# Optimization experiments

Hardware: AMD Instinct MI355X
Metric: run time of the kernel (lower is better)

## Reference

```python
import jax, jax.numpy as jnp
import numpy as np

B, T, C, L = 64, 1000, 128, 100  # batch, frames, classes (blank=C-1), max label len
NEG = jnp.float32(-1e30)


def setup_inputs() -> dict:
    key = jax.random.key(0)
    k0, k1, k2, k3 = jax.random.split(key, 4)
    # ctc_batch_cost expects softmax probabilities
    y_pred = jax.nn.softmax(jax.random.normal(k0, (B, T, C), dtype=jnp.float32), axis=-1)
    y_true = jax.random.randint(k1, (B, L), 0, C - 1).astype(jnp.int32)  # labels exclude blank
    label_lengths = jax.random.randint(k2, (B,), L // 2, L + 1).astype(jnp.int32)
    input_lengths = jax.random.randint(k3, (B,), T // 2, T + 1).astype(jnp.int32)
    return {"y_true": y_true, "y_pred": y_pred,
            "input_lengths": input_lengths, "label_lengths": label_lengths}


def _ctc_loss(y_true, y_pred, input_lengths, label_lengths):
    # Keras: logits = log(y_pred + epsilon), blank index = C-1
    logp = jnp.log(y_pred + 1e-7)                     # [B,T,C]
    blank = C - 1
    S = 2 * L + 1
    # extended label sequence: blank, l1, blank, l2, ..., blank  -> [B,S]
    ext = jnp.full((B, S), blank, dtype=jnp.int32).at[:, 1::2].set(y_true)
    # gather per-extended-position log probs: [B,T,S]
    logp_ext = jnp.take_along_axis(logp, jnp.broadcast_to(ext[:, None, :], (B, T, S)), axis=2)
    # skip (s-2) transition allowed when ext[s] != blank and ext[s] != ext[s-2]
    ext_m2 = jnp.concatenate([jnp.full((B, 2), blank, jnp.int32), ext[:, :-2]], axis=1)
    skip = (ext != blank) & (ext != ext_m2)           # [B,S]

    alpha0 = jnp.full((B, S), NEG, dtype=logp.dtype)
    alpha0 = alpha0.at[:, 0].set(logp_ext[:, 0, 0]).at[:, 1].set(logp_ext[:, 0, 1])

    def step(alpha, xs):
        lp_t, t = xs                                   # lp_t [B,S]
        a1 = jnp.concatenate([jnp.full((B, 1), NEG, alpha.dtype), alpha[:, :-1]], axis=1)
        a2 = jnp.concatenate([jnp.full((B, 2), NEG, alpha.dtype), alpha[:, :-2]], axis=1)
        a2 = jnp.where(skip, a2, NEG)
        new = jnp.logaddexp(jnp.logaddexp(alpha, a1), a2) + lp_t
        # freeze alpha past each sample's input length
        alpha = jnp.where(t < input_lengths[:, None], new, alpha)
        return alpha, None

    xs = (jnp.moveaxis(logp_ext, 1, 0)[1:], jnp.arange(1, T))
    alpha, _ = jax.lax.scan(step, alpha0, xs)
    # final positions: S_b-1 = 2*label_len, S_b-2 = 2*label_len - 1
    a_last = jnp.take_along_axis(alpha, (2 * label_lengths)[:, None], axis=1)[:, 0]
    a_prev = jnp.take_along_axis(alpha, (2 * label_lengths - 1)[:, None], axis=1)[:, 0]
    return -jnp.logaddexp(a_last, a_prev)[:, None]     # [B,1] like ctc_batch_cost


def reference(y_true, y_pred, input_lengths, label_lengths):
    return _ctc_loss(y_true, y_pred, input_lengths, label_lengths)
```

## Files before the change

kernel.cpp:

```cpp
#include <hip/hip_runtime.h>

#define B_ 64
#define T_ 1000
#define C_ 128
#define L_ 100
#define BLANK 127
#define LN2F 0.69314718055994530942f
#define PH 32
#define FSTRIDE 1024
#define BUFSZ (PH * FSTRIDE)

__device__ __forceinline__ float flog2(float x) { return __builtin_amdgcn_logf(x); }
__device__ __forceinline__ float frcp(float x)  { return __builtin_amdgcn_rcpf(x); }

#define DPP_ROW_SHR1   0x111
#define DPP_ROW_SHR2   0x112
#define DPP_ROW_SHR4   0x114
#define DPP_ROW_SHR8   0x118
#define DPP_WAVE_SHR1  0x138
#define DPP_WAVE_SHL1  0x130

template <int CTRL>
__device__ __forceinline__ int dpp_mov(int src) {
    return __builtin_amdgcn_update_dpp(0, src, CTRL, 0xF, 0xF, false);
}

__global__ __launch_bounds__(320) void ctc_split_kernel(
    const int* __restrict__ y_true, const float* __restrict__ y_pred,
    const int* __restrict__ in_len, const int* __restrict__ lab_len,
    double* __restrict__ AVf, double* __restrict__ AVb,
    double* __restrict__ Ls, int* __restrict__ Es)
{
    const int bb    = blockIdx.x & 63;
    const bool isB  = blockIdx.x >= 64;
    const int tid   = threadIdx.x;
    const int l     = tid & 63;
    const int wv    = tid >> 6;

    __shared__ __align__(16) char ldsb[2 * BUFSZ + 64];
    __shared__ float lgs[2][4];

    const int k1 = min(2 * l, L_ - 1);
    const int k3 = min(2 * l + 1, L_ - 1);
    const int e1 = y_true[bb * L_ + k1];
    const int e3 = y_true[bb * L_ + k3];
    const double m1 = (k1 == 0 || e1 != y_true[bb * L_ + k1 - 1]) ? 1.0 : 0.0;
    const double m3 = (e3 != y_true[bb * L_ + k3 - 1]) ? 1.0 : 0.0;
    const int k1n = min(2 * l + 2, L_ - 1);
    const double m1n = (y_true[bb * L_ + k1n] != y_true[bb * L_ + k1n - 1]) ? 1.0 : 0.0;

    const int Teff = min(T_, in_len[bb]);
    const int N    = Teff - 1;
    const int Hf   = (N + 1) >> 1;
    const int Hb   = N - Hf;
    const int steps_total = isB ? Hb : Hf;
    const int P_full = steps_total >> 5;
    const int rem    = steps_total & 31;
    const int P      = P_full + (rem ? 1 : 0);
    const float* rowb = y_pred + (size_t)bb * T_ * C_;

    double a0 = 0.0, a1 = 0.0, a2 = 0.0, a3 = 0.0;
    double Lsum = 0.0;
    int E = 0;

    const int fs = (wv - 1) * 8;

    auto fillw = [&](int phf) {
        char* bbw = ldsb + (phf & 1) * BUFSZ;
        const int kb_ = phf * PH + fs;
        float g10,g30,gb0, g11,g31,gb1, g12,g32,gb2, g13,g33,gb3,
              g14,g34,gb4, g15,g35,gb5, g16,g36,gb6, g17,g37,gb7;
        int t0_,t1_,t2_,t3_,t4_,t5_,t6_,t7_;
#define FR(i_) (isB ? (N - (kb_ + i_)) : (1 + kb_ + i_))
        t0_=FR(0); t1_=FR(1); t2_=FR(2); t3_=FR(3);
        t4_=FR(4); t5_=FR(5); t6_=FR(6); t7_=FR(7);
#undef FR
        {
            const float* r_;
            r_ = rowb + (size_t)min(max(t0_,1),N) * C_; g10=r_[e1]; g30=r_[e3]; gb0=r_[BLANK];
            r_ = rowb + (size_t)min(max(t1_,1),N) * C_; g11=r_[e1]; g31=r_[e3]; gb1=r_[BLANK];
            r_ = rowb + (size_t)min(max(t2_,1),N) * C_; g12=r_[e1]; g32=r_[e3]; gb2=r_[BLANK];
            r_ = rowb + (size_t)min(max(t3_,1),N) * C_; g13=r_[e1]; g33=r_[e3]; gb3=r_[BLANK];
            r_ = rowb + (size_t)min(max(t4_,1),N) * C_; g14=r_[e1]; g34=r_[e3]; gb4=r_[BLANK];
            r_ = rowb + (size_t)min(max(t5_,1),N) * C_; g15=r_[e1]; g35=r_[e3]; gb5=r_[BLANK];
            r_ = rowb + (size_t)min(max(t6_,1),N) * C_; g16=r_[e1]; g36=r_[e3]; gb6=r_[BLANK];
            r_ = rowb + (size_t)min(max(t7_,1),N) * C_; g17=r_[e1]; g37=r_[e3]; gb7=r_[BLANK];
        }
        __builtin_amdgcn_sched_barrier(0);
        float lgs_ = 0.f;
#define PWR(i_, T_V, G1, G3, GB) { \
        float rb_ = GB + 1e-7f; \
        float rc_ = frcp(rb_); \
        char* q_ = bbw + ((kb_ & 31) + i_) * FSTRIDE; \
        *(double2*)(q_ + 16 * l) = make_double2((double)((G1 + 1e-7f) * rc_), \
                                                 (double)((G3 + 1e-7f) * rc_)); \
        bool ok_ = isB ? (T_V >= Hf + 1 && T_V <= N) : (T_V >= 1 && T_V <= Hf); \
        lgs_ += ok_ ? flog2(rb_) : 0.f; }
        PWR(0, t0_, g10, g30, gb0); PWR(1, t1_, g11, g31, gb1);
        PWR(2, t2_, g12, g32, gb2); PWR(3, t3_, g13, g33, gb3);
        PWR(4, t4_, g14, g34, gb4); PWR(5, t5_, g15, g35, gb5);
        PWR(6, t6_, g16, g36, gb6); PWR(7, t7_, g17, g37, gb7);
#undef PWR
        if (l == 0) lgs[phf & 1][wv - 1] = lgs_;
    };

#define DECLF(Pr) double Pr##q1, Pr##q3
#define DECLB(Pr) double Pr##q1, Pr##q3, Pr##q1n
#define LDF(Pr, fi_) { \
    double2 v_ = *(const double2*)(bbp_ + (fi_) * FSTRIDE + 16 * l); \
    Pr##q1 = v_.x; Pr##q3 = v_.y; }
#define LDFB(Pr, fi_) { \
    double2 v_ = *(const double2*)(bbp_ + (fi_) * FSTRIDE + 16 * l); \
    Pr##q1 = v_.x; Pr##q3 = v_.y; \
    Pr##q1n = *(const double*)(bbp_ + (fi_) * FSTRIDE + 16 * ((l + 1) & 63)); }

#define STEPQ(Pr) { \
    int slo_ = dpp_mov<DPP_WAVE_SHR1>(__double2loint(a3)); \
    int shi_ = dpp_mov<DPP_WAVE_SHR1>(__double2hiint(a3)); \
    double pm1_ = __hiloint2double(shi_, slo_); \
    double n0_ = a0 + pm1_; \
    double n1_ = (a1 + a0 + m1 * pm1_) * Pr##q1; \
    double n2_ = a2 + a1; \
    double n3_ = (a3 + a2 + m3 * a1) * Pr##q3; \
    a0 = n0_; a1 = n1_; a2 = n2_; a3 = n3_; }

#define STEPB(Pr) { \
    int n0lo_ = dpp_mov<DPP_WAVE_SHL1>(__double2loint(a0)); \
    int n0hi_ = dpp_mov<DPP_WAVE_SHL1>(__double2hiint(a0)); \
    int n1lo_ = dpp_mov<DPP_WAVE_SHL1>(__double2loint(a1)); \
    int n1hi_ = dpp_mov<DPP_WAVE_SHL1>(__double2hiint(a1)); \
    double b0n_ = __hiloint2double(n0hi_, n0lo_); \
    double b1n_ = __hiloint2double(n1hi_, n1lo_); \
    double c1_ = a1 * Pr##q1; \
    double c3_ = a3 * Pr##q3; \
    double c1n_ = b1n_ * Pr##q1n; \
    double n0_ = a0 + c1_; \
    double n1_ = c1_ + a2 + m3 * c3_; \
    double n2_ = a2 + c3_; \
    double n3_ = c3_ + b0n_ + m1n * c1n_; \
    a0 = n0_; a1 = n1_; a2 = n2_; a3 = n3_; }

#define DPPMAX(u_, ctrl_) { unsigned t_ = (unsigned)dpp_mov<ctrl_>((int)(u_)); \
    u_ = max(u_, t_); }
#define RESCALE() { \
    unsigned u_ = max(max((unsigned)__double2hiint(a0), (unsigned)__double2hiint(a1)), \
                      max((unsigned)__double2hiint(a2), (unsigned)__double2hiint(a3))); \
    DPPMAX(u_, DPP_ROW_SHR1); \
    DPPMAX(u_, DPP_ROW_SHR2); \
    DPPMAX(u_, DPP_ROW_SHR4); \
    DPPMAX(u_, DPP_ROW_SHR8); \
    unsigned g_ = max(max((unsigned)__builtin_amdgcn_readlane((int)u_, 15), \
                          (unsigned)__builtin_amdgcn_readlane((int)u_, 31)), \
                      max((unsigned)__builtin_amdgcn_readlane((int)u_, 47), \
                          (unsigned)__builtin_amdgcn_readlane((int)u_, 63))); \
    int kk_ = (int)(g_ >> 20); \
    if (kk_ > 0) { \
        double f_ = __hiloint2double((2046 - kk_) << 20, 0); \
        a0 *= f_; a1 *= f_; a2 *= f_; a3 *= f_; \
        E += kk_ - 1023; } }

    if (wv >= 1) {
        fillw(0);
    } else if (!isB) {
        __builtin_amdgcn_s_setprio(1);
        float pb0_ = rowb[BLANK] + 1e-7f;
        float p10_ = rowb[e1]    + 1e-7f;
        a0 = (l == 0) ? 1.0 : 0.0;
        a1 = (l == 0) ? (double)(p10_ / pb0_) : 0.0;
        Lsum = (double)flog2(pb0_);
    } else {
        __builtin_amdgcn_s_setprio(1);
        const int llb = lab_len[bb];
        const int pa = 2 * llb, pq = 2 * llb - 1;
        a0 = (4 * l     == pa) ? 1.0 : 0.0;
        a1 = (4 * l + 1 == pq) ? 1.0 : 0.0;
        a2 = (4 * l + 2 == pa) ? 1.0 : 0.0;
        a3 = (4 * l + 3 == pq) ? 1.0 : 0.0;
    }
    __syncthreads();

    for (int ph = 0; ph < P; ++ph) {
        if (wv >= 1) {
            if (ph + 1 < P) fillw(ph + 1);
        } else {
            const char* bbp_ = ldsb + (ph & 1) * BUFSZ;
            const int steps = (ph < P_full) ? 32 : rem;
            if (!isB) {
                if (steps == 32) {
                    DECLF(A0); DECLF(A1); DECLF(A2); DECLF(A3);
                    DECLF(B0); DECLF(B1); DECLF(B2); DECLF(B3);
                    LDF(A0,0); LDF(A1,1); LDF(A2,2); LDF(A3,3);
                    LDF(B0,4); LDF(B1,5); LDF(B2,6); LDF(B3,7);
                    { STEPQ(A0); STEPQ(A1); STEPQ(A2); STEPQ(A3); }
                    LDF(A0,8); LDF(A1,9); LDF(A2,10); LDF(A3,11);
                    { STEPQ(B0); STEPQ(B1); STEPQ(B2); STEPQ(B3); }
                    LDF(B0,12); LDF(B1,13); LDF(B2,14); LDF(B3,15);
                    { STEPQ(A0); STEPQ(A1); STEPQ(A2); STEPQ(A3); }
                    LDF(A0,16); LDF(A1,17); LDF(A2,18); LDF(A3,19);
                    { STEPQ(B0); STEPQ(B1); STEPQ(B2); STEPQ(B3); } RESCALE();
                    LDF(B0,20); LDF(B1,21); LDF(B2,22); LDF(B3,23);
                    { STEPQ(A0); STEPQ(A1); STEPQ(A2); STEPQ(A3); }
                    LDF(A0,24); LDF(A1,25); LDF(A2,26); LDF(A3,27);
                    { STEPQ(B0); STEPQ(B1); STEPQ(B2); STEPQ(B3); }
                    LDF(B0,28); LDF(B1,29); LDF(B2,30); LDF(B3,31);
                    { STEPQ(A0); STEPQ(A1); STEPQ(A2); STEPQ(A3); }
                    { STEPQ(B0); STEPQ(B1); STEPQ(B2); STEPQ(B3); } RESCALE();
                } else {
                    for (int k_ = 0; k_ < steps; ++k_) {
                        DECLF(Tq); LDF(Tq, k_); STEPQ(Tq);
                        if (k_ == 15) RESCALE();
                    }
                    RESCALE();
                }
            } else {
                if (steps == 32) {
                    DECLB(A0); DECLB(A1); DECLB(A2); DECLB(A3);
                    DECLB(B0); DECLB(B1); DECLB(B2); DECLB(B3);
                    LDFB(A0,0); LDFB(A1,1); LDFB(A2,2); LDFB(A3,3);
                    LDFB(B0,4); LDFB(B1,5); LDFB(B2,6); LDFB(B3,7);
                    { STEPB(A0); STEPB(A1); STEPB(A2); STEPB(A3); }
                    LDFB(A0,8); LDFB(A1,9); LDFB(A2,10); LDFB(A3,11);
                    { STEPB(B0); STEPB(B1); STEPB(B2); STEPB(B3); }
                    LDFB(B0,12); LDFB(B1,13); LDFB(B2,14); LDFB(B3,15);
                    { STEPB(A0); STEPB(A1); STEPB(A2); STEPB(A3); }
                    LDFB(A0,16); LDFB(A1,17); LDFB(A2,18); LDFB(A3,19);
                    { STEPB(B0); STEPB(B1); STEPB(B2); STEPB(B3); } RESCALE();
                    LDFB(B0,20); LDFB(B1,21); LDFB(B2,22); LDFB(B3,23);
                    { STEPB(A0); STEPB(A1); STEPB(A2); STEPB(A3); }
                    LDFB(A0,24); LDFB(A1,25); LDFB(A2,26); LDFB(A3,27);
                    { STEPB(B0); STEPB(B1); STEPB(B2); STEPB(B3); }
                    LDFB(B0,28); LDFB(B1,29); LDFB(B2,30); LDFB(B3,31);
                    { STEPB(A0); STEPB(A1); STEPB(A2); STEPB(A3); }
                    { STEPB(B0); STEPB(B1); STEPB(B2); STEPB(B3); } RESCALE();
                } else {
                    for (int k_ = 0; k_ < steps; ++k_) {
                        DECLB(Tq); LDFB(Tq, k_); STEPB(Tq);
                        if (k_ == 15) RESCALE();
                    }
                    RESCALE();
                }
            }
            Lsum += (double)(lgs[ph & 1][0] + lgs[ph & 1][1] +
                             lgs[ph & 1][2] + lgs[ph & 1][3]);
        }
        __syncthreads();
    }

    if (wv == 0) {
        double* AV = (isB ? AVb : AVf) + bb * 256;
        AV[4 * l + 0] = a0; AV[4 * l + 1] = a1;
        AV[4 * l + 2] = a2; AV[4 * l + 3] = a3;
        if (l == 0) {
            Ls[bb * 2 + (isB ? 1 : 0)] = Lsum;
            Es[bb * 2 + (isB ? 1 : 0)] = E;
        }
    }
}

__global__ __launch_bounds__(64) void ctc_combine_kernel(
    const double* __restrict__ AVf, const double* __restrict__ AVb,
    const double* __restrict__ Ls, const int* __restrict__ Es,
    float* __restrict__ out)
{
    const int b = blockIdx.x;
    const int l = threadIdx.x;
    const double* f = AVf + b * 256;
    const double* g = AVb + b * 256;
    double d = f[4*l+0]*g[4*l+0] + f[4*l+1]*g[4*l+1]
             + f[4*l+2]*g[4*l+2] + f[4*l+3]*g[4*l+3];
    d += __shfl_xor(d, 1);  d += __shfl_xor(d, 2);  d += __shfl_xor(d, 4);
    d += __shfl_xor(d, 8);  d += __shfl_xor(d, 16); d += __shfl_xor(d, 32);
    if (l == 0) {
        double Ltot = Ls[b * 2] + Ls[b * 2 + 1];
        int    Etot = Es[b * 2] + Es[b * 2 + 1];
        int hi = __double2hiint(d), lo = __double2loint(d);
        int ke = (hi >> 20) & 0x7FF;
        double mant = __hiloint2double((hi & 0x000FFFFF) | (1023 << 20), lo);
        float r = flog2((float)mant) + (float)(ke - 1023 + Etot) + (float)Ltot;
        out[b] = -r * LN2F;
    }
}

extern "C" void kernel_launch(void* const* d_in, const int* in_sizes, int n_in,
                              void* d_out, int out_size, void* d_ws, size_t ws_size,
                              hipStream_t stream) {
    const int*   y_true  = (const int*)d_in[0];
    const float* y_pred  = (const float*)d_in[1];
    const int*   in_len  = (const int*)d_in[2];
    const int*   lab_len = (const int*)d_in[3];
    float*       out     = (float*)d_out;

    double* AVf = (double*)d_ws;
    double* AVb = AVf + 64 * 256;
    double* Ls  = AVb + 64 * 256;
    int*    Es  = (int*)(Ls + 128);

    ctc_split_kernel<<<128, 320, 0, stream>>>(y_true, y_pred, in_len, lab_len,
                                              AVf, AVb, Ls, Es);
    ctc_combine_kernel<<<64, 64, 0, stream>>>(AVf, AVb, Ls, Es, out);
}
```

Before: 34.80 us.

## Fuse pairs of CTC time steps into precomputed two-step transition matrices

Result: slower. 54.48 us (+56.5%).

```diff
diff --git a/kernel.cpp b/kernel.cpp
--- a/kernel.cpp
+++ b/kernel.cpp
@@ -6,9 +6,9 @@
 #define L_ 100
 #define BLANK 127
 #define LN2F 0.69314718055994530942f
-#define PH 32
-#define FSTRIDE 1024
-#define BUFSZ (PH * FSTRIDE)
+#define NPROD 4
+#define SLOTSZ 8192
+#define BUFSZ (8 * SLOTSZ)
 
 __device__ __forceinline__ float flog2(float x) { return __builtin_amdgcn_logf(x); }
 __device__ __forceinline__ float frcp(float x)  { return __builtin_amdgcn_rcpf(x); }
@@ -37,108 +37,156 @@
     const int l     = tid & 63;
     const int wv    = tid >> 6;
 
-    __shared__ __align__(16) char ldsb[2 * BUFSZ + 64];
-    __shared__ float lgs[2][4];
-
+    __shared__ __align__(16) char ldsb[2 * BUFSZ];
+    __shared__ float lgs[2][NPROD];
+
+    const int* yb = y_true + bb * L_;
     const int k1 = min(2 * l, L_ - 1);
     const int k3 = min(2 * l + 1, L_ - 1);
-    const int e1 = y_true[bb * L_ + k1];
-    const int e3 = y_true[bb * L_ + k3];
-    const double m1 = (k1 == 0 || e1 != y_true[bb * L_ + k1 - 1]) ? 1.0 : 0.0;
-    const double m3 = (e3 != y_true[bb * L_ + k3 - 1]) ? 1.0 : 0.0;
+    const int e1 = yb[k1];
+    const int e3 = yb[k3];
+    const float m1f  = (k1 == 0 || e1 != yb[k1 - 1]) ? 1.f : 0.f;
+    const float m3f  = (e3 != yb[k3 - 1]) ? 1.f : 0.f;
+    const int kp  = min(max(2 * l - 1, 1), L_ - 1);
+    const float mpf  = (yb[kp] != yb[kp - 1]) ? 1.f : 0.f;
     const int k1n = min(2 * l + 2, L_ - 1);
-    const double m1n = (y_true[bb * L_ + k1n] != y_true[bb * L_ + k1n - 1]) ? 1.0 : 0.0;
+    const float m1nf = (yb[k1n] != yb[k1n - 1]) ? 1.f : 0.f;
+    const int k3n = min(2 * l + 3, L_ - 1);
+    const float m3nf = (yb[k3n] != yb[k3n - 1]) ? 1.f : 0.f;
+    const int ep  = yb[min(max(2 * l - 1, 0), L_ - 1)];
+    const int e1n = yb[k1n];
+    const int e3n = yb[k3n];
 
     const int Teff = min(T_, in_len[bb]);
     const int N    = Teff - 1;
     const int Hf   = (N + 1) >> 1;
     const int Hb   = N - Hf;
     const int steps_total = isB ? Hb : Hf;
-    const int P_full = steps_total >> 5;
-    const int rem    = steps_total & 31;
-    const int P      = P_full + (rem ? 1 : 0);
+    const int ST   = (steps_total + 1) >> 1;
+    const int P    = (ST + 7) >> 3;
     const float* rowb = y_pred + (size_t)bb * T_ * C_;
 
     double a0 = 0.0, a1 = 0.0, a2 = 0.0, a3 = 0.0;
     double Lsum = 0.0;
     int E = 0;
 
-    const int fs = (wv - 1) * 8;
-
-    auto fillw = [&](int phf) {
-        char* bbw = ldsb + (phf & 1) * BUFSZ;
-        const int kb_ = phf * PH + fs;
-        float g10,g30,gb0, g11,g31,gb1, g12,g32,gb2, g13,g33,gb3,
-              g14,g34,gb4, g15,g35,gb5, g16,g36,gb6, g17,g37,gb7;
-        int t0_,t1_,t2_,t3_,t4_,t5_,t6_,t7_;
-#define FR(i_) (isB ? (N - (kb_ + i_)) : (1 + kb_ + i_))
-        t0_=FR(0); t1_=FR(1); t2_=FR(2); t3_=FR(3);
-        t4_=FR(4); t5_=FR(5); t6_=FR(6); t7_=FR(7);
-#undef FR
-        {
-            const float* r_;
-            r_ = rowb + (size_t)min(max(t0_,1),N) * C_; g10=r_[e1]; g30=r_[e3]; gb0=r_[BLANK];
-            r_ = rowb + (size_t)min(max(t1_,1),N) * C_; g11=r_[e1]; g31=r_[e3]; gb1=r_[BLANK];
-            r_ = rowb + (size_t)min(max(t2_,1),N) * C_; g12=r_[e1]; g32=r_[e3]; gb2=r_[BLANK];
-            r_ = rowb + (size_t)min(max(t3_,1),N) * C_; g13=r_[e1]; g33=r_[e3]; gb3=r_[BLANK];
-            r_ = rowb + (size_t)min(max(t4_,1),N) * C_; g14=r_[e1]; g34=r_[e3]; gb4=r_[BLANK];
-            r_ = rowb + (size_t)min(max(t5_,1),N) * C_; g15=r_[e1]; g35=r_[e3]; gb5=r_[BLANK];
-            r_ = rowb + (size_t)min(max(t6_,1),N) * C_; g16=r_[e1]; g36=r_[e3]; gb6=r_[BLANK];
-            r_ = rowb + (size_t)min(max(t7_,1),N) * C_; g17=r_[e1]; g37=r_[e3]; gb7=r_[BLANK];
+#define WRP(p_, X_, Y_) { *(double2*)(sbase + (p_) * 1024 + 16 * l) = \
+        make_double2((double)(X_), (double)(Y_)); }
+
+    auto fill_slot = [&](int ss, float& lgacc) {
+        char* sbase = ldsb + ((ss >> 3) & 1) * BUFSZ + (ss & 7) * SLOTSZ;
+        if (!isB) {
+            const int t1   = 2 * ss + 1;
+            const bool full = (2 * ss + 2 <= Hf);
+            const int t2   = full ? t1 + 1 : t1;
+            const float* r1 = rowb + (size_t)t1 * C_;
+            const float* r2 = rowb + (size_t)t2 * C_;
+            float p1a = r1[e1], p1b = r1[e3], p1p = r1[ep], b1v = r1[BLANK];
+            float p2a = r2[e1], p2b = r2[e3], b2v = r2[BLANK];
+            __builtin_amdgcn_sched_barrier(0);
+            float rc1 = frcp(b1v + 1e-7f), rc2 = frcp(b2v + 1e-7f);
+            float qa = (p1a + 1e-7f) * rc1, qb = (p1b + 1e-7f) * rc1,
+                  qp = (p1p + 1e-7f) * rc1;
+            float ra = (p2a + 1e-7f) * rc2, rb = (p2b + 1e-7f) * rc2;
+            float K01,K02,K03,K11,K12,K13,K14,K15,K21,K22,K23,K31,K32,K33,K34,K35;
+            if (full) {
+                K01 = 1.f + qp;  K02 = qp;  K03 = mpf * qp;
+                K11 = ra * qa;   K12 = ra * (qa + 1.f);
+                K13 = ra * (m1f * (qa + qp) + 1.f);
+                K14 = ra * m1f * qp;  K15 = K14 * mpf;
+                K21 = 1.f + qa;  K22 = qa;  K23 = m1f * qa;
+                K31 = rb * qb;   K32 = rb * (qb + 1.f);
+                K33 = rb * (m3f * (qb + qa) + 1.f);
+                K34 = rb * m3f * qa;  K35 = K34 * m1f;
+            } else {
+                K01 = 1.f; K02 = 0.f; K03 = 0.f;
+                K11 = qa;  K12 = qa;  K13 = m1f * qa; K14 = 0.f; K15 = 0.f;
+                K21 = 1.f; K22 = 0.f; K23 = 0.f;
+                K31 = qb;  K32 = qb;  K33 = m3f * qb; K34 = 0.f; K35 = 0.f;
+            }
+            WRP(0,K01,K02); WRP(1,K03,K11); WRP(2,K12,K13); WRP(3,K14,K15);
+            WRP(4,K21,K22); WRP(5,K23,K31); WRP(6,K32,K33); WRP(7,K34,K35);
+            lgacc += flog2(b1v + 1e-7f) + (full ? flog2(b2v + 1e-7f) : 0.f);
+        } else {
+            const int fR   = N - 2 * ss;
+            const bool full = (2 * ss + 2 <= Hb);
+            const int fQ   = full ? fR - 1 : fR;
+            const float* rQ = rowb + (size_t)fQ * C_;
+            const float* rR = rowb + (size_t)fR * C_;
+            float gqa = rQ[e1], gqb = rQ[e3], gqan = rQ[e1n], bQ = rQ[BLANK];
+            float gra = rR[e1], grb = rR[e3], gran = rR[e1n], grbn = rR[e3n],
+                  bR  = rR[BLANK];
+            __builtin_amdgcn_sched_barrier(0);
+            float rcQ = frcp(bQ + 1e-7f), rcR = frcp(bR + 1e-7f);
+            float qa1  = (gqa  + 1e-7f) * rcQ, qb1  = (gqb  + 1e-7f) * rcQ,
+                  qa1n = (gqan + 1e-7f) * rcQ;
+            float ra2  = (gra  + 1e-7f) * rcR, rb2  = (grb  + 1e-7f) * rcR,
+                  ra2n = (gran + 1e-7f) * rcR, rb2n = (grbn + 1e-7f) * rcR;
+            float T01,T02,T03,T11,T12,T13,T14,T15,T21,T22,T23,T31,T32,T33,T34,T35;
+            if (full) {
+                T01 = ra2 * (qa1 + 1.f); T02 = qa1; T03 = rb2 * m3f * qa1;
+                T11 = ra2 * qa1; T12 = 1.f + qa1;
+                T13 = rb2 * (m3f * (qb1 + qa1) + 1.f);
+                T14 = m3f * qb1; T15 = ra2n * m1nf * T14;
+                T21 = rb2 * (qb1 + 1.f); T22 = qb1; T23 = ra2n * m1nf * qb1;
+                T31 = rb2 * qb1; T32 = 1.f + qb1;
+                T33 = ra2n * (m1nf * (qa1n + qb1) + 1.f);
+                T34 = m1nf * qa1n; T35 = rb2n * m3nf * T34;
+            } else {
+                T01 = ra2; T02 = 0.f; T03 = 0.f;
+                T11 = ra2; T12 = 1.f; T13 = m3f * rb2; T14 = 0.f; T15 = 0.f;
+                T21 = rb2; T22 = 0.f; T23 = 0.f;
+                T31 = rb2; T32 = 1.f; T33 = m1nf * ra2n; T34 = 0.f; T35 = 0.f;
+            }
+            WRP(0,T01,T02); WRP(1,T03,T11); WRP(2,T12,T13); WRP(3,T14,T15);
+            WRP(4,T21,T22); WRP(5,T23,T31); WRP(6,T32,T33); WRP(7,T34,T35);
+            lgacc += flog2(bR + 1e-7f) + (full ? flog2(bQ + 1e-7f) : 0.f);
         }
-        __builtin_amdgcn_sched_barrier(0);
-        float lgs_ = 0.f;
-#define PWR(i_, T_V, G1, G3, GB) { \
-        float rb_ = GB + 1e-7f; \
-        float rc_ = frcp(rb_); \
-        char* q_ = bbw + ((kb_ & 31) + i_) * FSTRIDE; \
-        *(double2*)(q_ + 16 * l) = make_double2((double)((G1 + 1e-7f) * rc_), \
-                                                 (double)((G3 + 1e-7f) * rc_)); \
-        bool ok_ = isB ? (T_V >= Hf + 1 && T_V <= N) : (T_V >= 1 && T_V <= Hf); \
-        lgs_ += ok_ ? flog2(rb_) : 0.f; }
-        PWR(0, t0_, g10, g30, gb0); PWR(1, t1_, g11, g31, gb1);
-        PWR(2, t2_, g12, g32, gb2); PWR(3, t3_, g13, g33, gb3);
-        PWR(4, t4_, g14, g34, gb4); PWR(5, t5_, g15, g35, gb5);
-        PWR(6, t6_, g16, g36, gb6); PWR(7, t7_, g17, g37, gb7);
-#undef PWR
-        if (l == 0) lgs[phf & 1][wv - 1] = lgs_;
     };
 
-#define DECLF(Pr) double Pr##q1, Pr##q3
-#define DECLB(Pr) double Pr##q1, Pr##q3, Pr##q1n
-#define LDF(Pr, fi_) { \
-    double2 v_ = *(const double2*)(bbp_ + (fi_) * FSTRIDE + 16 * l); \
-    Pr##q1 = v_.x; Pr##q3 = v_.y; }
-#define LDFB(Pr, fi_) { \
-    double2 v_ = *(const double2*)(bbp_ + (fi_) * FSTRIDE + 16 * l); \
-    Pr##q1 = v_.x; Pr##q3 = v_.y; \
-    Pr##q1n = *(const double*)(bbp_ + (fi_) * FSTRIDE + 16 * ((l + 1) & 63)); }
-
-#define STEPQ(Pr) { \
-    int slo_ = dpp_mov<DPP_WAVE_SHR1>(__double2loint(a3)); \
-    int shi_ = dpp_mov<DPP_WAVE_SHR1>(__double2hiint(a3)); \
-    double pm1_ = __hiloint2double(shi_, slo_); \
-    double n0_ = a0 + pm1_; \
-    double n1_ = (a1 + a0 + m1 * pm1_) * Pr##q1; \
-    double n2_ = a2 + a1; \
-    double n3_ = (a3 + a2 + m3 * a1) * Pr##q3; \
-    a0 = n0_; a1 = n1_; a2 = n2_; a3 = n3_; }
-
-#define STEPB(Pr) { \
-    int n0lo_ = dpp_mov<DPP_WAVE_SHL1>(__double2loint(a0)); \
-    int n0hi_ = dpp_mov<DPP_WAVE_SHL1>(__double2hiint(a0)); \
-    int n1lo_ = dpp_mov<DPP_WAVE_SHL1>(__double2loint(a1)); \
-    int n1hi_ = dpp_mov<DPP_WAVE_SHL1>(__double2hiint(a1)); \
-    double b0n_ = __hiloint2double(n0hi_, n0lo_); \
-    double b1n_ = __hiloint2double(n1hi_, n1lo_); \
-    double c1_ = a1 * Pr##q1; \
-    double c3_ = a3 * Pr##q3; \
-    double c1n_ = b1n_ * Pr##q1n; \
-    double n0_ = a0 + c1_; \
-    double n1_ = c1_ + a2 + m3 * c3_; \
-    double n2_ = a2 + c3_; \
-    double n3_ = c3_ + b0n_ + m1n * c1n_; \
-    a0 = n0_; a1 = n1_; a2 = n2_; a3 = n3_; }
+    auto fill_phase = [&](int phf) {
+        float lg_ = 0.f;
+        const int s0 = phf * 8 + (wv - 1) * 2;
+        if (s0     < ST) fill_slot(s0,     lg_);
+        if (s0 + 1 < ST) fill_slot(s0 + 1, lg_);
+        if (l == 0) lgs[phf & 1][wv - 1] = lg_;
+    };
+
+#define DECLP(BK) double2 BK##0,BK##1,BK##2,BK##3,BK##4,BK##5,BK##6,BK##7
+#define LDP(BK, k_) { const char* sb_ = base_ + (k_) * SLOTSZ + 16 * l; \
+    BK##0 = *(const double2*)(sb_);        BK##1 = *(const double2*)(sb_ + 1024); \
+    BK##2 = *(const double2*)(sb_ + 2048); BK##3 = *(const double2*)(sb_ + 3072); \
+    BK##4 = *(const double2*)(sb_ + 4096); BK##5 = *(const double2*)(sb_ + 5120); \
+    BK##6 = *(const double2*)(sb_ + 6144); BK##7 = *(const double2*)(sb_ + 7168); }
+
+#define APPLYF(BK) { \
+    int l1_ = dpp_mov<DPP_WAVE_SHR1>(__double2loint(a1)), h1_ = dpp_mov<DPP_WAVE_SHR1>(__double2hiint(a1)); \
+    int l2_ = dpp_mov<DPP_WAVE_SHR1>(__double2loint(a2)), h2_ = dpp_mov<DPP_WAVE_SHR1>(__double2hiint(a2)); \
+    int l3_ = dpp_mov<DPP_WAVE_SHR1>(__double2loint(a3)), h3_ = dpp_mov<DPP_WAVE_SHR1>(__double2hiint(a3)); \
+    double pa1_ = __hiloint2double(h1_, l1_), pa2_ = __hiloint2double(h2_, l2_), \
+           pa3_ = __hiloint2double(h3_, l3_); \
+    double c0_ = fma((BK##0).x, pa3_, a0); c0_ = fma((BK##0).y, pa2_, c0_); c0_ = fma((BK##1).x, pa1_, c0_); \
+    double c1_ = (BK##1).y * a1; c1_ = fma((BK##2).x, a0, c1_); c1_ = fma((BK##2).y, pa3_, c1_); \
+    c1_ = fma((BK##3).x, pa2_, c1_); c1_ = fma((BK##3).y, pa1_, c1_); \
+    double c2_ = fma((BK##4).x, a1, a2); c2_ = fma((BK##4).y, a0, c2_); c2_ = fma((BK##5).x, pa3_, c2_); \
+    double c3_ = (BK##5).y * a3; c3_ = fma((BK##6).x, a2, c3_); c3_ = fma((BK##6).y, a1, c3_); \
+    c3_ = fma((BK##7).x, a0, c3_); c3_ = fma((BK##7).y, pa3_, c3_); \
+    a0 = c0_; a1 = c1_; a2 = c2_; a3 = c3_; }
+
+#define APPLYB(BK) { \
+    int l0_ = dpp_mov<DPP_WAVE_SHL1>(__double2loint(a0)), h0_ = dpp_mov<DPP_WAVE_SHL1>(__double2hiint(a0)); \
+    int l1_ = dpp_mov<DPP_WAVE_SHL1>(__double2loint(a1)), h1_ = dpp_mov<DPP_WAVE_SHL1>(__double2hiint(a1)); \
+    int l2_ = dpp_mov<DPP_WAVE_SHL1>(__double2loint(a2)), h2_ = dpp_mov<DPP_WAVE_SHL1>(__double2hiint(a2)); \
+    int l3_ = dpp_mov<DPP_WAVE_SHL1>(__double2loint(a3)), h3_ = dpp_mov<DPP_WAVE_SHL1>(__double2hiint(a3)); \
+    double nb0_ = __hiloint2double(h0_, l0_), nb1_ = __hiloint2double(h1_, l1_), \
+           nb2_ = __hiloint2double(h2_, l2_), nb3_ = __hiloint2double(h3_, l3_); \
+    double t0_ = fma((BK##0).x, a1, a0); t0_ = fma((BK##0).y, a2, t0_); t0_ = fma((BK##1).x, a3, t0_); \
+    double t1_ = (BK##1).y * a1; t1_ = fma((BK##2).x, a2, t1_); t1_ = fma((BK##2).y, a3, t1_); \
+    t1_ = fma((BK##3).x, nb0_, t1_); t1_ = fma((BK##3).y, nb1_, t1_); \
+    double t2_ = fma((BK##4).x, a3, a2); t2_ = fma((BK##4).y, nb0_, t2_); t2_ = fma((BK##5).x, nb1_, t2_); \
+    double t3_ = (BK##5).y * a3; t3_ = fma((BK##6).x, nb0_, t3_); t3_ = fma((BK##6).y, nb1_, t3_); \
+    t3_ = fma((BK##7).x, nb2_, t3_); t3_ = fma((BK##7).y, nb3_, t3_); \
+    a0 = t0_; a1 = t1_; a2 = t2_; a3 = t3_; }
 
 #define DPPMAX(u_, ctrl_) { unsigned t_ = (unsigned)dpp_mov<ctrl_>((int)(u_)); \
     u_ = max(u_, t_); }
@@ -160,7 +208,7 @@
         E += kk_ - 1023; } }
 
     if (wv >= 1) {
-        fillw(0);
+        fill_phase(0);
     } else if (!isB) {
         __builtin_amdgcn_s_setprio(1);
         float pb0_ = rowb[BLANK] + 1e-7f;
@@ -181,67 +229,37 @@
 
     for (int ph = 0; ph < P; ++ph) {
         if (wv >= 1) {
-            if (ph + 1 < P) fillw(ph + 1);
+            if (ph + 1 < P) fill_phase(ph + 1);
         } else {
-            const char* bbp_ = ldsb + (ph & 1) * BUFSZ;
-            const int steps = (ph < P_full) ? 32 : rem;
-            if (!isB) {
-                if (steps == 32) {
-                    DECLF(A0); DECLF(A1); DECLF(A2); DECLF(A3);
-                    DECLF(B0); DECLF(B1); DECLF(B2); DECLF(B3);
-                    LDF(A0,0); LDF(A1,1); LDF(A2,2); LDF(A3,3);
-                    LDF(B0,4); LDF(B1,5); LDF(B2,6); LDF(B3,7);
-                    { STEPQ(A0); STEPQ(A1); STEPQ(A2); STEPQ(A3); }
-                    LDF(A0,8); LDF(A1,9); LDF(A2,10); LDF(A3,11);
-                    { STEPQ(B0); STEPQ(B1); STEPQ(B2); STEPQ(B3); }
-                    LDF(B0,12); LDF(B1,13); LDF(B2,14); LDF(B3,15);
-                    { STEPQ(A0); STEPQ(A1); STEPQ(A2); STEPQ(A3); }
-                    LDF(A0,16); LDF(A1,17); LDF(A2,18); LDF(A3,19);
-                    { STEPQ(B0); STEPQ(B1); STEPQ(B2); STEPQ(B3); } RESCALE();
-                    LDF(B0,20); LDF(B1,21); LDF(B2,22); LDF(B3,23);
-                    { STEPQ(A0); STEPQ(A1); STEPQ(A2); STEPQ(A3); }
-                    LDF(A0,24); LDF(A1,25); LDF(A2,26); LDF(A3,27);
-                    { STEPQ(B0); STEPQ(B1); STEPQ(B2); STEPQ(B3); }
-                    LDF(B0,28); LDF(B1,29); LDF(B2,30); LDF(B3,31);
-                    { STEPQ(A0); STEPQ(A1); STEPQ(A2); STEPQ(A3); }
-                    { STEPQ(B0); STEPQ(B1); STEPQ(B2); STEPQ(B3); } RESCALE();
+            const char* base_ = ldsb + (ph & 1) * BUFSZ;
+            const int sp = min(8, ST - ph * 8);
+            if (sp == 8) {
+                DECLP(A); DECLP(B);
+                LDP(A, 0); LDP(B, 1);
+                if (!isB) {
+                    APPLYF(A); LDP(A, 2); APPLYF(B); LDP(B, 3);
+                    APPLYF(A); LDP(A, 4); APPLYF(B); LDP(B, 5);
+                    APPLYF(A); LDP(A, 6); APPLYF(B); LDP(B, 7);
+                    APPLYF(A); APPLYF(B);
                 } else {
-                    for (int k_ = 0; k_ < steps; ++k_) {
-                        DECLF(Tq); LDF(Tq, k_); STEPQ(Tq);
-                        if (k_ == 15) RESCALE();
-                    }
-                    RESCALE();
+                    APPLYB(A); LDP(A, 2); APPLYB(B); LDP(B, 3);
+                    APPLYB(A); LDP(A, 4); APPLYB(B); LDP(B, 5);
+                    APPLYB(A); LDP(A, 6); APPLYB(B); LDP(B, 7);
+                    APPLYB(A); APPLYB(B);
                 }
+                RESCALE();
             } else {
-                if (steps == 32) {
-                    DECLB(A0); DECLB(A1); DECLB(A2); DECLB(A3);
-                    DECLB(B0); DECLB(B1); DECLB(B2); DECLB(B3);
-                    LDFB(A0,0); LDFB(A1,1); LDFB(A2,2); LDFB(A3,3);
-                    LDFB(B0,4); LDFB(B1,5); LDFB(B2,6); LDFB(B3,7);
-                    { STEPB(A0); STEPB(A1); STEPB(A2); STEPB(A3); }
-                    LDFB(A0,8); LDFB(A1,9); LDFB(A2,10); LDFB(A3,11);
-                    { STEPB(B0); STEPB(B1); STEPB(B2); STEPB(B3); }
-                    LDFB(B0,12); LDFB(B1,13); LDFB(B2,14); LDFB(B3,15);
-                    { STEPB(A0); STEPB(A1); STEPB(A2); STEPB(A3); }
-                    LDFB(A0,16); LDFB(A1,17); LDFB(A2,18); LDFB(A3,19);
-                    { STEPB(B0); STEPB(B1); STEPB(B2); STEPB(B3); } RESCALE();
-                    LDFB(B0,20); LDFB(B1,21); LDFB(B2,22); LDFB(B3,23);
-                    { STEPB(A0); STEPB(A1); STEPB(A2); STEPB(A3); }
-                    LDFB(A0,24); LDFB(A1,25); LDFB(A2,26); LDFB(A3,27);
-                    { STEPB(B0); STEPB(B1); STEPB(B2); STEPB(B3); }
-                    LDFB(B0,28); LDFB(B1,29); LDFB(B2,30); LDFB(B3,31);
-                    { STEPB(A0); STEPB(A1); STEPB(A2); STEPB(A3); }
-                    { STEPB(B0); STEPB(B1); STEPB(B2); STEPB(B3); } RESCALE();
-                } else {
-                    for (int k_ = 0; k_ < steps; ++k_) {
-                        DECLB(Tq); LDFB(Tq, k_); STEPB(Tq);
-                        if (k_ == 15) RESCALE();
-                    }
-                    RESCALE();
+                for (int k_ = 0; k_ < sp; ++k_) {
+                    DECLP(Tt);
+                    LDP(Tt, k_);
+                    if (!isB) { APPLYF(Tt); } else { APPLYB(Tt); }
                 }
+                RESCALE();
             }
-            Lsum += (double)(lgs[ph & 1][0] + lgs[ph & 1][1] +
-                             lgs[ph & 1][2] + lgs[ph & 1][3]);
+            float lg_ = 0.f;
+            #pragma unroll
+            for (int w_ = 0; w_ < NPROD; ++w_) lg_ += lgs[ph & 1][w_];
+            Lsum += (double)lg_;
         }
         __syncthreads();
     }
```
